# Performance work log

Hardware: AMD Instinct MI355X
Metric: run time of the kernel (lower is better)

Reference implementation:

```python
import jax, jax.numpy as jnp
import numpy as np

B = 131072
FLOW_SIZE = 16
PASS = 8
TRANS = FLOW_SIZE - PASS  # 8
N_BINS = 128
HIDDEN = 256


def setup_inputs() -> dict:
    key = jax.random.key(0)
    k0, k1, k2 = jax.random.split(key, 3)
    x = jax.random.uniform(k0, (B, FLOW_SIZE + 1), dtype=jnp.float32)
    W1 = jax.random.normal(k1, (PASS, HIDDEN), dtype=jnp.float32) * 0.3
    b1 = jnp.zeros((HIDDEN,), dtype=jnp.float32)
    W2 = jax.random.normal(k2, (HIDDEN, TRANS * N_BINS), dtype=jnp.float32) * 0.05
    b2 = jnp.zeros((TRANS * N_BINS,), dtype=jnp.float32)
    return {"x": x, "W1": W1, "b1": b1, "W2": W2, "b2": b2}


def reference(x, W1, b1, W2, b2):
    xA = x[:, :PASS]                      # [B, P]
    xB = x[:, PASS:FLOW_SIZE]             # [B, T]
    jacobian = x[:, FLOW_SIZE:FLOW_SIZE + 1]  # [B, 1]

    # NN: small MLP, exp output -> positive unnormalized bin widths Q [B, T, n_bins]
    h = jax.nn.relu(xA @ W1 + b1)
    Q = jnp.exp(h @ W2 + b2).reshape(x.shape[0], TRANS, N_BINS)

    Qsum = jnp.cumsum(Q, axis=-1)                     # [B, T, n_bins]
    Qnorms = Qsum[:, :, -1:]                          # [B, T, 1]
    Q = Q / (Qnorms / N_BINS)                         # normalized slopes
    Qsum = Qsum / Qnorms                              # normalized CDF
    Qsum = jnp.pad(Qsum, ((0, 0), (0, 0), (1, 0)))    # left-pad CDF with 0

    alphas = xB * N_BINS
    bins = jnp.floor(alphas)
    alphas = (alphas - bins) / N_BINS                 # fractional offset within bin
    bins = jnp.clip(bins.astype(jnp.int32), 0, N_BINS - 1)

    cdf_int_part = jnp.take_along_axis(Qsum, bins[..., None], axis=-1)[..., 0]  # [B, T]
    cdf_float_part = jnp.take_along_axis(Q, bins[..., None], axis=-1)[..., 0]   # [B, T]

    cdf = cdf_float_part * alphas + cdf_int_part      # [B, T]
    jacobian = jacobian * jnp.prod(cdf_float_part, axis=-1, keepdims=True)  # [B, 1]

    return jnp.concatenate((xA, cdf, jacobian), axis=-1)  # [B, flow_size+1]
```

## Files before the change

kernel.cpp:

```cpp
#include <hip/hip_runtime.h>
#include <math.h>

#define NROWS 131072
#define XC    17
#define ROWSB 128
#define HID   256
#define NB    128
#define NCOL  1024
#define LOG2E 1.44269504088896340736f

typedef __attribute__((ext_vector_type(8))) short bf16x8;
typedef __attribute__((ext_vector_type(4))) float f32x4;

__device__ __forceinline__ unsigned short f2bf(float f) {
    unsigned int u = __float_as_uint(f);
    return (unsigned short)((u + 0x7FFFu + ((u >> 16) & 1u)) >> 16);
}

__device__ __forceinline__ float red16(float v) {
    int x;
    x = __builtin_amdgcn_update_dpp(0, __float_as_int(v), 0xB1, 0xF, 0xF, true);
    v += __int_as_float(x);
    x = __builtin_amdgcn_update_dpp(0, __float_as_int(v), 0x4E, 0xF, 0xF, true);
    v += __int_as_float(x);
    x = __builtin_amdgcn_update_dpp(0, __float_as_int(v), 0x141, 0xF, 0xF, true);
    v += __int_as_float(x);
    x = __builtin_amdgcn_update_dpp(0, __float_as_int(v), 0x140, 0xF, 0xF, true);
    v += __int_as_float(x);
    return v;
}

__global__ void prep_w2(const float* __restrict__ W2, unsigned short* __restrict__ w2t) {
    const int g   = blockIdx.x * 256 + threadIdx.x;
    const int col = g >> 5, go = g & 31;
    const int kg  = (go & ~7) | ((go & 7) ^ (col & 7));
    unsigned int p[4];
    #pragma unroll
    for (int j = 0; j < 4; ++j) {
        const unsigned short lo = f2bf(W2[(size_t)(kg * 8 + 2 * j) * NCOL + col] * LOG2E);
        const unsigned short hi = f2bf(W2[(size_t)(kg * 8 + 2 * j + 1) * NCOL + col] * LOG2E);
        p[j] = (unsigned int)lo | ((unsigned int)hi << 16);
    }
    *(uint4*)&w2t[(size_t)col * HID + go * 8] = make_uint4(p[0], p[1], p[2], p[3]);
}

__global__ __launch_bounds__(256, 2)
void gplc4(const float* __restrict__ x,
           const float* __restrict__ W1,
           const float* __restrict__ b1,
           const unsigned short* __restrict__ w2t,
           const float* __restrict__ b2,
           float* __restrict__ out)
{
    __shared__ float xs[ROWSB * XC];
    __shared__ __align__(16) union {
        unsigned short hb[ROWSB * HID];
        struct { unsigned short w2[2][NB * 64]; float b2s[NCOL]; } g;
    } u;

    const int tid  = threadIdx.x;
    const int lane = tid & 63;
    const int w    = tid >> 6;
    const int quad = lane >> 4;
    const int l15  = lane & 15;
    const int wr   = w * 32;
    const int ksw  = (lane & 7) << 3;
    const size_t r0 = (size_t)blockIdx.x * ROWSB;

    for (int i = tid; i < ROWSB * XC; i += 256) xs[i] = x[r0 * XC + i];
    const int cp = tid & 127, hlf = tid >> 7;
    float w1r[16];
    #pragma unroll
    for (int i = 0; i < 8; ++i) {
        const float2 t2 = *(const float2*)&W1[i * HID + 2 * cp];
        w1r[2 * i] = t2.x; w1r[2 * i + 1] = t2.y;
    }
    const float2 b1v = *(const float2*)&b1[2 * cp];
    __syncthreads();

    for (int r = 0; r < 64; ++r) {
        const int row = hlf * 64 + r;
        float a0 = b1v.x, a1 = b1v.y;
        #pragma unroll
        for (int i = 0; i < 8; ++i) {
            const float xv = xs[row * XC + i];
            a0 = fmaf(xv, w1r[2 * i], a0);
            a1 = fmaf(xv, w1r[2 * i + 1], a1);
        }
        a0 = fmaxf(a0, 0.f); a1 = fmaxf(a1, 0.f);
        const int eidx = row * HID + (((cp >> 2) ^ (row & 15)) << 3) + ((cp & 3) << 1);
        *(unsigned int*)&u.hb[eidx] = (unsigned int)f2bf(a0) | ((unsigned int)f2bf(a1) << 16);
    }
    __syncthreads();

    bf16x8 afr[2][8];
    #pragma unroll
    for (int rt = 0; rt < 2; ++rt)
        #pragma unroll
        for (int kf = 0; kf < 8; ++kf) {
            const int row = wr + rt * 16 + l15;
            afr[rt][kf] = *(const bf16x8*)&u.hb[row * HID + (((kf * 4 + quad) ^ l15) << 3)];
        }
    __syncthreads();

    for (int i = tid; i < NCOL; i += 256) u.g.b2s[i] = b2[i] * LOG2E;

    auto stage = [&](int n) {
        const int t = n >> 2, kc = n & 3, buf = n & 1;
        #pragma unroll
        for (int j = 0; j < 4; ++j) {
            const int ob = (w * 4 + j) * 512;
            const int c  = (ob >> 6) + (lane >> 3);
            const int kl = (lane & 7) << 3;
            const unsigned short* gp = w2t + (size_t)(t * NB + c) * HID + kc * 64 + kl;
            unsigned short* lp = &u.g.w2[buf][ob];
            __builtin_amdgcn_global_load_lds(
                (const __attribute__((address_space(1))) unsigned int*)gp,
                (__attribute__((address_space(3))) unsigned int*)lp, 16, 0, 0);
        }
    };

    float jf[2][4] = {{1.f,1.f,1.f,1.f},{1.f,1.f,1.f,1.f}};

    stage(0);
    #pragma unroll 1
    for (int t = 0; t < 8; ++t) {
        f32x4 acc[2][8];
        #pragma unroll
        for (int rt = 0; rt < 2; ++rt)
            #pragma unroll
            for (int ct = 0; ct < 8; ++ct) acc[rt][ct] = (f32x4){0.f, 0.f, 0.f, 0.f};

        #pragma unroll
        for (int kc = 0; kc < 4; ++kc) {
            __syncthreads();
            const int n = t * 4 + kc;
            if (n < 31) stage(n + 1);
            const unsigned short* wsb = u.g.w2[kc & 1];
            #pragma unroll
            for (int ks = 0; ks < 2; ++ks) {
                const int kf = kc * 2 + ks;
                const int klog = ks * 32 + quad * 8;
                #pragma unroll
                for (int ct = 0; ct < 8; ++ct) {
                    const int c = ct * 16 + l15;
                    const bf16x8 bf = *(const bf16x8*)&wsb[c * 64 + (klog ^ ksw)];
                    acc[0][ct] = __builtin_amdgcn_mfma_f32_16x16x32_bf16(afr[0][kf], bf, acc[0][ct], 0, 0, 0);
                    acc[1][ct] = __builtin_amdgcn_mfma_f32_16x16x32_bf16(afr[1][kf], bf, acc[1][ct], 0, 0, 0);
                }
            }
        }

        float bb[8];
        #pragma unroll
        for (int ct = 0; ct < 8; ++ct) bb[ct] = u.g.b2s[t * NB + ct * 16 + l15];
        #pragma unroll
        for (int rt = 0; rt < 2; ++rt)
            #pragma unroll
            for (int i = 0; i < 4; ++i) {
                const int row = wr + rt * 16 + quad * 4 + i;
                const float alpha = xs[row * XC + 8 + t] * 128.f;
                const float fb = floorf(alpha);
                const int bin = min(max((int)fb, 0), 127);
                const float fr = alpha - fb;
                float tot = 0.f, num = 0.f, eb = 0.f;
                #pragma unroll
                for (int ct = 0; ct < 8; ++ct) {
                    const int col = ct * 16 + l15;
                    const float e = exp2f(acc[rt][ct][i] + bb[ct]);
                    tot += e;
                    num += (col < bin)  ? e : 0.f;
                    eb  += (col == bin) ? e : 0.f;
                }
                tot = red16(tot); num = red16(num); eb = red16(eb);
                const float inv = 1.f / tot;
                jf[rt][i] *= 128.f * eb * inv;
                if (l15 == 0) xs[row * XC + 8 + t] = fmaf(eb, fr, num) * inv;
            }
    }

    if (l15 == 0) {
        #pragma unroll
        for (int rt = 0; rt < 2; ++rt)
            #pragma unroll
            for (int i = 0; i < 4; ++i) {
                const int row = wr + rt * 16 + quad * 4 + i;
                xs[row * XC + 16] *= jf[rt][i];
            }
    }
    __syncthreads();
    for (int i = tid; i < ROWSB * XC; i += 256) out[r0 * XC + i] = xs[i];
}

extern "C" void kernel_launch(void* const* d_in, const int* in_sizes, int n_in,
                              void* d_out, int out_size, void* d_ws, size_t ws_size,
                              hipStream_t stream) {
    (void)in_sizes; (void)n_in; (void)ws_size; (void)out_size;
    prep_w2<<<(NCOL * HID / 8) / 256, 256, 0, stream>>>(
        (const float*)d_in[3], (unsigned short*)d_ws);
    gplc4<<<NROWS / ROWSB, 256, 0, stream>>>(
        (const float*)d_in[0], (const float*)d_in[1], (const float*)d_in[2],
        (const unsigned short*)d_ws, (const float*)d_in[4], (float*)d_out);
}
```

Before: 195.0 us.

## Split bin columns across wave pairs, defer cross-wave CDF combine via LDS

Each wave now computes 64 rows by 64 bin columns instead of 32 rows by 128 columns. Each B-fragment read from LDS therefore feeds four MFMAs instead of two, which halves the shared-memory traffic for W2. The per-row partial sums (total, below-bin, at-bin) are written to an LDS scratch array, and 128 threads combine them one iteration later, overlapped with the next GEMM. The masked epilogue sums become prefix-sum selects, and fast hardware exp2/rcp intrinsics replace the library calls. A-fragment registers double, which may raise register pressure and cut occupancy.

```diff
diff --git a/kernel.cpp b/kernel.cpp
--- a/kernel.cpp
+++ b/kernel.cpp
@@ -11,6 +11,17 @@
 
 typedef __attribute__((ext_vector_type(8))) short bf16x8;
 typedef __attribute__((ext_vector_type(4))) float f32x4;
+
+#if __has_builtin(__builtin_amdgcn_exp2f)
+#define EXP2F(v) __builtin_amdgcn_exp2f(v)
+#else
+#define EXP2F(v) exp2f(v)
+#endif
+#if __has_builtin(__builtin_amdgcn_rcpf)
+#define RCPF(v) __builtin_amdgcn_rcpf(v)
+#else
+#define RCPF(v) (1.f / (v))
+#endif
 
 __device__ __forceinline__ unsigned short f2bf(float f) {
     unsigned int u = __float_as_uint(f);
@@ -45,7 +56,7 @@
 }
 
 __global__ __launch_bounds__(256, 2)
-void gplc4(const float* __restrict__ x,
+void gplc7(const float* __restrict__ x,
            const float* __restrict__ W1,
            const float* __restrict__ b1,
            const unsigned short* __restrict__ w2t,
@@ -53,6 +64,7 @@
            float* __restrict__ out)
 {
     __shared__ float xs[ROWSB * XC];
+    __shared__ float red[ROWSB][2][3];
     __shared__ __align__(16) union {
         unsigned short hb[ROWSB * HID];
         struct { unsigned short w2[2][NB * 64]; float b2s[NCOL]; } g;
@@ -63,7 +75,8 @@
     const int w    = tid >> 6;
     const int quad = lane >> 4;
     const int l15  = lane & 15;
-    const int wr   = w * 32;
+    const int grp  = w >> 1;
+    const int half = w & 1;
     const int ksw  = (lane & 7) << 3;
     const size_t r0 = (size_t)blockIdx.x * ROWSB;
 
@@ -93,12 +106,12 @@
     }
     __syncthreads();
 
-    bf16x8 afr[2][8];
+    bf16x8 afr[4][8];
     #pragma unroll
-    for (int rt = 0; rt < 2; ++rt)
+    for (int rt = 0; rt < 4; ++rt)
         #pragma unroll
         for (int kf = 0; kf < 8; ++kf) {
-            const int row = wr + rt * 16 + l15;
+            const int row = grp * 64 + rt * 16 + l15;
             afr[rt][kf] = *(const bf16x8*)&u.hb[row * HID + (((kf * 4 + quad) ^ l15) << 3)];
         }
     __syncthreads();
@@ -120,73 +133,99 @@
         }
     };
 
-    float jf[2][4] = {{1.f,1.f,1.f,1.f},{1.f,1.f,1.f,1.f}};
+    float jfr = 1.f;
 
     stage(0);
     #pragma unroll 1
     for (int t = 0; t < 8; ++t) {
-        f32x4 acc[2][8];
-        #pragma unroll
-        for (int rt = 0; rt < 2; ++rt)
+        f32x4 acc[4][4];
+        #pragma unroll
+        for (int rt = 0; rt < 4; ++rt)
             #pragma unroll
-            for (int ct = 0; ct < 8; ++ct) acc[rt][ct] = (f32x4){0.f, 0.f, 0.f, 0.f};
+            for (int ct = 0; ct < 4; ++ct) acc[rt][ct] = (f32x4){0.f, 0.f, 0.f, 0.f};
 
         #pragma unroll
         for (int kc = 0; kc < 4; ++kc) {
             __syncthreads();
             const int n = t * 4 + kc;
             if (n < 31) stage(n + 1);
+            if (kc == 0 && t > 0 && tid < ROWSB) {
+                const int tf = t - 1;
+                const float tot = red[tid][0][0] + red[tid][1][0];
+                const float num = red[tid][0][1] + red[tid][1][1];
+                const float eb  = red[tid][0][2] + red[tid][1][2];
+                const float alpha = xs[tid * XC + 8 + tf] * 128.f;
+                const float fr  = alpha - floorf(alpha);
+                const float inv = RCPF(tot);
+                xs[tid * XC + 8 + tf] = fmaf(eb, fr, num) * inv;
+                jfr *= 128.f * eb * inv;
+            }
             const unsigned short* wsb = u.g.w2[kc & 1];
             #pragma unroll
             for (int ks = 0; ks < 2; ++ks) {
                 const int kf = kc * 2 + ks;
                 const int klog = ks * 32 + quad * 8;
                 #pragma unroll
-                for (int ct = 0; ct < 8; ++ct) {
-                    const int c = ct * 16 + l15;
+                for (int ct = 0; ct < 4; ++ct) {
+                    const int c = half * 64 + ct * 16 + l15;
                     const bf16x8 bf = *(const bf16x8*)&wsb[c * 64 + (klog ^ ksw)];
                     acc[0][ct] = __builtin_amdgcn_mfma_f32_16x16x32_bf16(afr[0][kf], bf, acc[0][ct], 0, 0, 0);
                     acc[1][ct] = __builtin_amdgcn_mfma_f32_16x16x32_bf16(afr[1][kf], bf, acc[1][ct], 0, 0, 0);
+                    acc[2][ct] = __builtin_amdgcn_mfma_f32_16x16x32_bf16(afr[2][kf], bf, acc[2][ct], 0, 0, 0);
+                    acc[3][ct] = __builtin_amdgcn_mfma_f32_16x16x32_bf16(afr[3][kf], bf, acc[3][ct], 0, 0, 0);
                 }
             }
         }
 
-        float bb[8];
-        #pragma unroll
-        for (int ct = 0; ct < 8; ++ct) bb[ct] = u.g.b2s[t * NB + ct * 16 + l15];
-        #pragma unroll
-        for (int rt = 0; rt < 2; ++rt)
+        float bb[4];
+        #pragma unroll
+        for (int ct = 0; ct < 4; ++ct)
+            bb[ct] = u.g.b2s[t * NB + half * 64 + ct * 16 + l15];
+        #pragma unroll
+        for (int rt = 0; rt < 4; ++rt)
             #pragma unroll
             for (int i = 0; i < 4; ++i) {
-                const int row = wr + rt * 16 + quad * 4 + i;
+                const int row = grp * 64 + rt * 16 + quad * 4 + i;
                 const float alpha = xs[row * XC + 8 + t] * 128.f;
                 const float fb = floorf(alpha);
                 const int bin = min(max((int)fb, 0), 127);
-                const float fr = alpha - fb;
-                float tot = 0.f, num = 0.f, eb = 0.f;
-                #pragma unroll
-                for (int ct = 0; ct < 8; ++ct) {
-                    const int col = ct * 16 + l15;
-                    const float e = exp2f(acc[rt][ct][i] + bb[ct]);
-                    tot += e;
-                    num += (col < bin)  ? e : 0.f;
-                    eb  += (col == bin) ? e : 0.f;
+                float e0 = EXP2F(acc[rt][0][i] + bb[0]);
+                float e1 = EXP2F(acc[rt][1][i] + bb[1]);
+                float e2 = EXP2F(acc[rt][2][i] + bb[2]);
+                float e3 = EXP2F(acc[rt][3][i] + bb[3]);
+                const float P1 = e0, P2 = P1 + e1, P3 = P2 + e2, P4 = P3 + e3;
+                int thr = (bin - half * 64 - l15 + 15) >> 4;
+                thr = min(max(thr, 0), 4);
+                const float sa = (thr & 1) ? P1 : 0.f;
+                const float sb = (thr & 1) ? P3 : P2;
+                const float sn = (thr & 2) ? sb : sa;
+                float num = (thr >= 4) ? P4 : sn;
+                const int cb = (bin >> 4) & 3;
+                const float ea = (cb & 1) ? e1 : e0;
+                const float ec = (cb & 1) ? e3 : e2;
+                const float es = (cb & 2) ? ec : ea;
+                float eb  = (((bin >> 6) == half) && ((bin & 15) == l15)) ? es : 0.f;
+                float tot = P4;
+                tot = red16(tot); num = red16(num); eb = red16(eb);
+                if (l15 == 0) {
+                    red[row][half][0] = tot;
+                    red[row][half][1] = num;
+                    red[row][half][2] = eb;
                 }
-                tot = red16(tot); num = red16(num); eb = red16(eb);
-                const float inv = 1.f / tot;
-                jf[rt][i] *= 128.f * eb * inv;
-                if (l15 == 0) xs[row * XC + 8 + t] = fmaf(eb, fr, num) * inv;
             }
     }
 
-    if (l15 == 0) {
-        #pragma unroll
-        for (int rt = 0; rt < 2; ++rt)
-            #pragma unroll
-            for (int i = 0; i < 4; ++i) {
-                const int row = wr + rt * 16 + quad * 4 + i;
-                xs[row * XC + 16] *= jf[rt][i];
-            }
+    __syncthreads();
+    if (tid < ROWSB) {
+        const float tot = red[tid][0][0] + red[tid][1][0];
+        const float num = red[tid][0][1] + red[tid][1][1];
+        const float eb  = red[tid][0][2] + red[tid][1][2];
+        const float alpha = xs[tid * XC + 15] * 128.f;
+        const float fr  = alpha - floorf(alpha);
+        const float inv = RCPF(tot);
+        xs[tid * XC + 15] = fmaf(eb, fr, num) * inv;
+        jfr *= 128.f * eb * inv;
+        xs[tid * XC + 16] *= jfr;
     }
     __syncthreads();
     for (int i = tid; i < ROWSB * XC; i += 256) out[r0 * XC + i] = xs[i];
@@ -198,7 +237,7 @@
     (void)in_sizes; (void)n_in; (void)ws_size; (void)out_size;
     prep_w2<<<(NCOL * HID / 8) / 256, 256, 0, stream>>>(
         (const float*)d_in[3], (unsigned short*)d_ws);
-    gplc4<<<NROWS / ROWSB, 256, 0, stream>>>(
+    gplc7<<<NROWS / ROWSB, 256, 0, stream>>>(
         (const float*)d_in[0], (const float*)d_in[1], (const float*)d_in[2],
         (const unsigned short*)d_ws, (const float*)d_in[4], (float*)d_out);
 }
```

After: 208.7 us. 1.07x slower.
